# Kernel optimization log

Hardware: AMD Instinct MI355X
Metric: run time of the kernel (lower is better)

Reference implementation:

```python
import jax, jax.numpy as jnp
import numpy as np

N = 10000       # atoms
E = 160000      # edges
F = 128         # node_dim
NB = 20         # num radial basis
BLOCKS = 3      # action_blocks
CUTOFF = 5.0
ZMAX = 100
EPS = 1e-8


def _layernorm(x, g, b):
    mu = jnp.mean(x, axis=-1, keepdims=True)
    var = jnp.var(x, axis=-1, keepdims=True)
    return (x - mu) * jax.lax.rsqrt(var + 1e-5) * g + b


def setup_inputs() -> dict:
    key = jax.random.key(0)
    ks = jax.random.split(key, 16)
    W = 0.05  # weight init scale, keeps activations stable over 3 blocks
    inp = {
        "pos": jax.random.uniform(ks[0], (N, 3), dtype=jnp.float32),
        "z": jax.random.randint(ks[1], (N,), 0, ZMAX),
        "edge_index": jax.random.randint(ks[2], (2, E), 0, N),
        "z_embed": jax.random.normal(ks[3], (ZMAX, F), dtype=jnp.float32),
        "Wrbf": jax.random.normal(ks[4], (BLOCKS, NB, 3 * F), dtype=jnp.float32) * W,
        "brbf": jnp.zeros((BLOCKS, 3 * F), jnp.float32),
        "ln_g": jnp.ones((BLOCKS, F), jnp.float32),
        "ln_b": jnp.zeros((BLOCKS, F), jnp.float32),
        "Wm1": jax.random.normal(ks[5], (BLOCKS, F, F), dtype=jnp.float32) * W,
        "bm1": jnp.zeros((BLOCKS, F), jnp.float32),
        "Wm2": jax.random.normal(ks[6], (BLOCKS, F, 3 * F), dtype=jnp.float32) * W,
        "bm2": jnp.zeros((BLOCKS, 3 * F), jnp.float32),
        "Uw": jax.random.normal(ks[7], (BLOCKS, F, F), dtype=jnp.float32) * W,
        "Vw": jax.random.normal(ks[8], (BLOCKS, F, F), dtype=jnp.float32) * W,
        "ln2_g": jnp.ones((BLOCKS, F), jnp.float32),
        "ln2_b": jnp.zeros((BLOCKS, F), jnp.float32),
        "Wu1": jax.random.normal(ks[9], (BLOCKS, 2 * F, F), dtype=jnp.float32) * W,
        "bu1": jnp.zeros((BLOCKS, F), jnp.float32),
        "Wu2": jax.random.normal(ks[10], (BLOCKS, F, 3 * F), dtype=jnp.float32) * W,
        "bu2": jnp.zeros((BLOCKS, 3 * F), jnp.float32),
        "Wo1": jax.random.normal(ks[11], (F, F), dtype=jnp.float32) * W,
        "bo1": jnp.zeros((F,), jnp.float32),
        "Wo2": jax.random.normal(ks[12], (F, 1), dtype=jnp.float32) * W,
        "bo2": jnp.zeros((1,), jnp.float32),
    }
    return inp


def _forward(pos, z, edge_index, z_embed, Wrbf, brbf, ln_g, ln_b, Wm1, bm1,
             Wm2, bm2, Uw, Vw, ln2_g, ln2_b, Wu1, bu1, Wu2, bu2,
             Wo1, bo1, Wo2, bo2):
    src, dst = edge_index[0], edge_index[1]
    # ---- edge data: distances, bessel RBF, cosine cutoff ----
    rvec = pos[dst] - pos[src]                          # [E,3]
    d = jnp.sqrt(jnp.sum(rvec * rvec, axis=-1) + EPS)   # [E]
    rhat = rvec / d[:, None]                            # [E,3]
    n = jnp.arange(1, NB + 1, dtype=jnp.float32)
    rbf = jnp.sin(n[None, :] * jnp.pi * d[:, None] / CUTOFF) / d[:, None]  # [E,NB]
    fc = jnp.where(d < CUTOFF, 0.5 * (jnp.cos(jnp.pi * d / CUTOFF) + 1.0), 0.0)
    # ---- embedding ----
    x = z_embed[z]                                      # [N,F] scalar features
    v = jnp.zeros((x.shape[0], 3, F), x.dtype)          # [N,3,F] vector features
    nseg = x.shape[0]
    for b in range(BLOCKS):
        # ---- message block (PaiNN) ----
        xn = _layernorm(x, ln_g[b], ln_b[b])
        phi = jax.nn.silu(xn @ Wm1[b] + bm1[b]) @ Wm2[b] + bm2[b]          # [N,3F]
        Wf = (rbf @ Wrbf[b] + brbf[b]) * fc[:, None]                       # [E,3F]
        m = phi[src] * Wf                                                  # [E,3F]
        ms, mvv, mvs = m[:, :F], m[:, F:2 * F], m[:, 2 * F:]
        dx = jax.ops.segment_sum(ms, dst, num_segments=nseg)               # [N,F]
        ev = mvv[:, None, :] * v[src] + mvs[:, None, :] * rhat[:, :, None] # [E,3,F]
        dv = jax.ops.segment_sum(ev, dst, num_segments=nseg)               # [N,3,F]
        x = x + dx
        v = v + dv
        # ---- update block (PaiNN) ----
        Uv = jnp.einsum('ncf,fg->ncg', v, Uw[b])
        Vv = jnp.einsum('ncf,fg->ncg', v, Vw[b])
        vnorm = jnp.sqrt(jnp.sum(Vv * Vv, axis=1) + EPS)                   # [N,F]
        xn2 = _layernorm(x, ln2_g[b], ln2_b[b])
        a = jax.nn.silu(jnp.concatenate([xn2, vnorm], -1) @ Wu1[b] + bu1[b]) @ Wu2[b] + bu2[b]
        avv, asv, ass = a[:, :F], a[:, F:2 * F], a[:, 2 * F:]
        x = x + asv * jnp.sum(Uv * Vv, axis=1) + ass
        v = v + avv[:, None, :] * Uv
    # ---- energy output head ----
    e_atom = jax.nn.silu(x @ Wo1 + bo1) @ Wo2 + bo2                        # [N,1]
    return jnp.sum(e_atom)


def reference(pos, z, edge_index, z_embed, Wrbf, brbf, ln_g, ln_b, Wm1, bm1,
              Wm2, bm2, Uw, Vw, ln2_g, ln2_b, Wu1, bu1, Wu2, bu2,
              Wo1, bo1, Wo2, bo2):
    return _forward(pos, z, edge_index, z_embed, Wrbf, brbf, ln_g, ln_b,
                    Wm1, bm1, Wm2, bm2, Uw, Vw, ln2_g, ln2_b,
                    Wu1, bu1, Wu2, bu2, Wo1, bo1, Wo2, bo2)
```

## Files before the change

kernel.cpp:

```cpp
#include <hip/hip_runtime.h>
#include <math.h>

#define N_ATOM 10000
#define NEDGE  160000
#define F      128
#define F3     384
#define NB     20
#define NBLK   3
#define PI_F   3.14159265358979323846f

__device__ __forceinline__ float silu_f(float x){ return x / (1.0f + __expf(-x)); }

__global__ __launch_bounds__(256) void k_init(const float* __restrict__ z_embed,
                                              const int* __restrict__ z,
                                              float* __restrict__ x, float* __restrict__ v){
  int idx = blockIdx.x * 256 + threadIdx.x;
  if (idx < N_ATOM * F){
    int i = idx >> 7, f = idx & 127;
    x[idx] = z_embed[z[i] * F + f];
  }
  if (idx < N_ATOM * 3 * F) v[idx] = 0.0f;
}

__global__ __launch_bounds__(256) void k_hist(const int* __restrict__ ei, int* __restrict__ deg){
  int e = blockIdx.x * 256 + threadIdx.x;
  atomicAdd(&deg[ei[NEDGE + e]], 1);
}

__global__ __launch_bounds__(1024) void k_scan(const int* __restrict__ deg,
                                               int* __restrict__ rowptr, int* __restrict__ cursor){
  __shared__ int part[1024];
  int t = threadIdx.x;
  int base = t * 10;
  int loc[10];
  int s = 0;
  #pragma unroll
  for (int i = 0; i < 10; i++){
    int idx = base + i;
    int d = (idx < N_ATOM) ? deg[idx] : 0;
    loc[i] = s; s += d;
  }
  part[t] = s;
  __syncthreads();
  for (int off = 1; off < 1024; off <<= 1){
    int vp = 0;
    if (t >= off) vp = part[t - off];
    __syncthreads();
    part[t] += vp;
    __syncthreads();
  }
  int offset = (t == 0) ? 0 : part[t - 1];
  #pragma unroll
  for (int i = 0; i < 10; i++){
    int idx = base + i;
    if (idx < N_ATOM){ rowptr[idx] = offset + loc[i]; cursor[idx] = offset + loc[i]; }
  }
  if (t == 1023) rowptr[N_ATOM] = part[1023];
}

__global__ __launch_bounds__(256) void k_slot(const int* __restrict__ ei,
                                              int* __restrict__ cursor, int* __restrict__ slot){
  int e = blockIdx.x * 256 + threadIdx.x;
  int p = atomicAdd(&cursor[ei[NEDGE + e]], 1);
  slot[e] = p;
}

__global__ __launch_bounds__(256) void k_geo(const float* __restrict__ pos,
                                             const int* __restrict__ ei,
                                             const int* __restrict__ slot,
                                             int* __restrict__ srcs,
                                             float* __restrict__ rhs,
                                             float* __restrict__ rbfs,
                                             float* __restrict__ fcs){
  int e = blockIdx.x * 256 + threadIdx.x;
  int s = ei[e], d_ = ei[NEDGE + e];
  int p = slot[e];
  float rx = pos[d_*3+0] - pos[s*3+0];
  float ry = pos[d_*3+1] - pos[s*3+1];
  float rz = pos[d_*3+2] - pos[s*3+2];
  float d  = sqrtf(rx*rx + ry*ry + rz*rz + 1e-8f);
  float inv = 1.0f / d;
  srcs[p] = s;
  rhs[p*3+0] = rx*inv; rhs[p*3+1] = ry*inv; rhs[p*3+2] = rz*inv;
  float fcv = (d < 5.0f) ? 0.5f * (cosf(PI_F * d * 0.2f) + 1.0f) : 0.0f;
  fcs[p] = fcv;
  float base = PI_F * d * 0.2f;
  float sc = inv * fcv;
  #pragma unroll
  for (int k = 0; k < NB; k++){
    rbfs[(size_t)p*NB + k] = sinf(base * (float)(k+1)) * sc;
  }
}

__global__ __launch_bounds__(256) void k_node_phi(const float* __restrict__ x,
                                                  float* __restrict__ phi,
                                                  const float* __restrict__ ln_g, const float* __restrict__ ln_b,
                                                  const float* __restrict__ Wm1, const float* __restrict__ bm1,
                                                  const float* __restrict__ Wm2, const float* __restrict__ bm2){
  __shared__ float xn[16][F];
  __shared__ float h [16][F];
  __shared__ float mu_s[16], rs_s[16];
  int t = threadIdx.x;
  int row0 = blockIdx.x * 16;

  {
    int r = t >> 4, l = t & 15;
    const float* xr = x + (size_t)(row0 + r) * F;
    float s = 0.f, ss = 0.f;
    #pragma unroll
    for (int i = 0; i < 8; i++){ float vv = xr[l + 16*i]; s += vv; ss += vv*vv; }
    #pragma unroll
    for (int m = 8; m >= 1; m >>= 1){ s += __shfl_xor(s, m, 64); ss += __shfl_xor(ss, m, 64); }
    if (l == 0){
      float mu = s * (1.0f/F);
      float var = ss * (1.0f/F) - mu*mu;
      mu_s[r] = mu; rs_s[r] = rsqrtf(var + 1e-5f);
    }
  }
  __syncthreads();
  #pragma unroll
  for (int i = 0; i < 8; i++){
    int idx = t + 256*i; int r = idx >> 7, f = idx & 127;
    float vv = x[(size_t)(row0 + r)*F + f];
    xn[r][f] = (vv - mu_s[r]) * rs_s[r] * ln_g[f] + ln_b[f];
  }
  __syncthreads();
  {
    int c = t & 127, grp = t >> 7;
    float acc[8];
    #pragma unroll
    for (int i = 0; i < 8; i++) acc[i] = bm1[c];
    for (int k = 0; k < F; k++){
      float w = Wm1[k*F + c];
      #pragma unroll
      for (int i = 0; i < 8; i++) acc[i] += xn[grp*8 + i][k] * w;
    }
    #pragma unroll
    for (int i = 0; i < 8; i++) h[grp*8 + i][c] = silu_f(acc[i]);
  }
  __syncthreads();
  {
    int j = t & 127, grp = t >> 7;
    float a0[8], a1[8], a2[8];
    #pragma unroll
    for (int i = 0; i < 8; i++){ a0[i] = bm2[j]; a1[i] = bm2[128+j]; a2[i] = bm2[256+j]; }
    for (int k = 0; k < F; k++){
      float w0 = Wm2[k*F3 + j], w1 = Wm2[k*F3 + 128 + j], w2 = Wm2[k*F3 + 256 + j];
      #pragma unroll
      for (int i = 0; i < 8; i++){
        float hv = h[grp*8 + i][k];
        a0[i] += hv*w0; a1[i] += hv*w1; a2[i] += hv*w2;
      }
    }
    #pragma unroll
    for (int i = 0; i < 8; i++){
      size_t row = row0 + grp*8 + i;
      phi[row*F3 + j]       = a0[i];
      phi[row*F3 + 128 + j] = a1[i];
      phi[row*F3 + 256 + j] = a2[i];
    }
  }
}

__global__ __launch_bounds__(256) void k_edge_g(const int* __restrict__ rowptr,
                                                const int* __restrict__ srcs,
                                                const float* __restrict__ rbfs,
                                                const float* __restrict__ rhs,
                                                const float* __restrict__ fcs,
                                                const float* __restrict__ phi,
                                                const float* __restrict__ v,
                                                const float* __restrict__ Wrbf,
                                                const float* __restrict__ brbf,
                                                float* __restrict__ x,
                                                float* __restrict__ vnew){
  __shared__ float W[NB * F3];
  int t = threadIdx.x;
  #pragma unroll
  for (int i = 0; i < (NB*F3)/256; i++) W[t + 256*i] = Wrbf[t + 256*i];
  __syncthreads();

  int wid = t >> 6, lane = t & 63;
  int n = blockIdx.x * 4 + wid;
  int f0 = lane, f1 = lane + 64;
  int r0 = rowptr[n], r1 = rowptr[n+1];

  float bs0  = brbf[f0],       bs1  = brbf[f1];
  float bvv0 = brbf[F + f0],   bvv1 = brbf[F + f1];
  float bvs0 = brbf[2*F + f0], bvs1 = brbf[2*F + f1];

  float ax0=0.f, ax1=0.f;
  float av00=0.f, av01=0.f, av10=0.f, av11=0.f, av20=0.f, av21=0.f;

  for (int j = r0; j < r1; ++j){
    int s = srcs[j];
    float fcv = fcs[j];
    float rh0 = rhs[j*3+0], rh1 = rhs[j*3+1], rh2 = rhs[j*3+2];
    const float* rb = rbfs + (size_t)j * NB;
    float w_s0=0.f, w_s1=0.f, wvv0=0.f, wvv1=0.f, wvs0=0.f, wvs1=0.f;
    #pragma unroll
    for (int k = 0; k < NB; k++){
      float r = rb[k];
      w_s0 += r * W[k*F3 + f0];        w_s1 += r * W[k*F3 + f1];
      wvv0 += r * W[k*F3 + F + f0];    wvv1 += r * W[k*F3 + F + f1];
      wvs0 += r * W[k*F3 + 2*F + f0];  wvs1 += r * W[k*F3 + 2*F + f1];
    }
    const float* ps = phi + (size_t)s * F3;
    const float* vs = v   + (size_t)s * 3 * F;
    float ms0  = ps[f0]       * (w_s0 + bs0 *fcv);
    float ms1  = ps[f1]       * (w_s1 + bs1 *fcv);
    float mvv0 = ps[F + f0]   * (wvv0 + bvv0*fcv);
    float mvv1 = ps[F + f1]   * (wvv1 + bvv1*fcv);
    float mvs0 = ps[2*F + f0] * (wvs0 + bvs0*fcv);
    float mvs1 = ps[2*F + f1] * (wvs1 + bvs1*fcv);
    ax0 += ms0; ax1 += ms1;
    av00 += mvv0*vs[f0]       + mvs0*rh0;  av01 += mvv1*vs[f1]       + mvs1*rh0;
    av10 += mvv0*vs[F + f0]   + mvs0*rh1;  av11 += mvv1*vs[F + f1]   + mvs1*rh1;
    av20 += mvv0*vs[2*F + f0] + mvs0*rh2;  av21 += mvv1*vs[2*F + f1] + mvs1*rh2;
  }

  size_t xb = (size_t)n * F;
  x[xb + f0] += ax0;  x[xb + f1] += ax1;
  size_t vb = (size_t)n * 3 * F;
  vnew[vb + f0]       = v[vb + f0]       + av00;  vnew[vb + f1]       = v[vb + f1]       + av01;
  vnew[vb + F + f0]   = v[vb + F + f0]   + av10;  vnew[vb + F + f1]   = v[vb + F + f1]   + av11;
  vnew[vb + 2*F + f0] = v[vb + 2*F + f0] + av20;  vnew[vb + 2*F + f1] = v[vb + 2*F + f1] + av21;
}

__global__ __launch_bounds__(256) void k_node_upd(float* __restrict__ x, float* __restrict__ v,
                                                  const float* __restrict__ vnew,
                                                  const float* __restrict__ Uw, const float* __restrict__ Vw,
                                                  const float* __restrict__ ln2_g, const float* __restrict__ ln2_b,
                                                  const float* __restrict__ Wu1, const float* __restrict__ bu1,
                                                  const float* __restrict__ Wu2, const float* __restrict__ bu2){
  __shared__ float vn [8][3][F];
  __shared__ float Uvs[8][3][F];
  __shared__ float xl [8][F];
  __shared__ float xn2[8][F];
  __shared__ float vno[8][F];
  __shared__ float duv[8][F];
  __shared__ float hl [8][F];
  __shared__ float mu_s[8], rs_s[8];
  int t = threadIdx.x;
  int n0 = blockIdx.x * 8;

  #pragma unroll
  for (int i = 0; i < 12; i++){
    int idx = t + 256*i;
    ((float*)vn)[idx] = vnew[(size_t)n0*3*F + idx];
  }
  #pragma unroll
  for (int i = 0; i < 4; i++){
    int idx = t + 256*i;
    ((float*)xl)[idx] = x[(size_t)n0*F + idx];
  }
  __syncthreads();

  {
    int r = t >> 5, l = t & 31;
    float s = 0.f, ss = 0.f;
    #pragma unroll
    for (int i = 0; i < 4; i++){ float vv = xl[r][l + 32*i]; s += vv; ss += vv*vv; }
    #pragma unroll
    for (int m = 16; m >= 1; m >>= 1){ s += __shfl_xor(s, m, 64); ss += __shfl_xor(ss, m, 64); }
    if (l == 0){ float mu = s*(1.0f/F); mu_s[r] = mu; rs_s[r] = rsqrtf(ss*(1.0f/F) - mu*mu + 1e-5f); }
  }
  __syncthreads();
  #pragma unroll
  for (int i = 0; i < 4; i++){
    int idx = t + 256*i; int r = idx >> 7, f = idx & 127;
    xn2[r][f] = (xl[r][f] - mu_s[r]) * rs_s[r] * ln2_g[f] + ln2_b[f];
  }

  {
    int g = t & 127, grp = t >> 7;
    float au[12], av[12];
    #pragma unroll
    for (int p = 0; p < 12; p++){ au[p]=0.f; av[p]=0.f; }
    for (int k = 0; k < F; k++){
      float uw = Uw[k*F + g], vw = Vw[k*F + g];
      #pragma unroll
      for (int n = 0; n < 4; n++){
        #pragma unroll
        for (int c = 0; c < 3; c++){
          float vv = vn[grp*4 + n][c][k];
          au[n*3+c] += vv*uw; av[n*3+c] += vv*vw;
        }
      }
    }
    #pragma unroll
    for (int n = 0; n < 4; n++){
      float v0 = av[n*3+0], v1 = av[n*3+1], v2 = av[n*3+2];
      float u0 = au[n*3+0], u1 = au[n*3+1], u2 = au[n*3+2];
      vno[grp*4+n][g] = sqrtf(v0*v0 + v1*v1 + v2*v2 + 1e-8f);
      duv[grp*4+n][g] = u0*v0 + u1*v1 + u2*v2;
      Uvs[grp*4+n][0][g] = u0; Uvs[grp*4+n][1][g] = u1; Uvs[grp*4+n][2][g] = u2;
    }
  }
  __syncthreads();

  {
    int g = t & 127, grp = t >> 7;
    float acc[4];
    #pragma unroll
    for (int n = 0; n < 4; n++) acc[n] = bu1[g];
    for (int k = 0; k < F; k++){
      float w = Wu1[k*F + g];
      #pragma unroll
      for (int n = 0; n < 4; n++) acc[n] += xn2[grp*4+n][k] * w;
    }
    for (int k = 0; k < F; k++){
      float w = Wu1[(F + k)*F + g];
      #pragma unroll
      for (int n = 0; n < 4; n++) acc[n] += vno[grp*4+n][k] * w;
    }
    #pragma unroll
    for (int n = 0; n < 4; n++) hl[grp*4+n][g] = silu_f(acc[n]);
  }
  __syncthreads();

  {
    int f = t & 127, grp = t >> 7;
    float a0[4], a1[4], a2[4];
    #pragma unroll
    for (int n = 0; n < 4; n++){ a0[n] = bu2[f]; a1[n] = bu2[128+f]; a2[n] = bu2[256+f]; }
    for (int k = 0; k < F; k++){
      float w0 = Wu2[k*F3 + f], w1 = Wu2[k*F3 + 128 + f], w2 = Wu2[k*F3 + 256 + f];
      #pragma unroll
      for (int n = 0; n < 4; n++){
        float hv = hl[grp*4+n][k];
        a0[n] += hv*w0; a1[n] += hv*w1; a2[n] += hv*w2;
      }
    }
    #pragma unroll
    for (int n = 0; n < 4; n++){
      int nl = grp*4 + n;
      size_t row = n0 + nl;
      x[row*F + f] = xl[nl][f] + a1[n]*duv[nl][f] + a2[n];
      #pragma unroll
      for (int c = 0; c < 3; c++)
        v[(row*3 + c)*F + f] = vn[nl][c][f] + a0[n]*Uvs[nl][c][f];
    }
  }
}

__global__ __launch_bounds__(256) void k_out(const float* __restrict__ x,
                                             const float* __restrict__ Wo1, const float* __restrict__ bo1,
                                             const float* __restrict__ Wo2, const float* __restrict__ bo2,
                                             float* __restrict__ out){
  __shared__ float xl[8][F];
  __shared__ float hl[8][F];
  __shared__ float er[8];
  int t = threadIdx.x; int n0 = blockIdx.x * 8;
  #pragma unroll
  for (int i = 0; i < 4; i++){ int idx = t + 256*i; ((float*)xl)[idx] = x[(size_t)n0*F + idx]; }
  __syncthreads();
  { int g = t & 127, grp = t >> 7;
    float acc[4];
    #pragma unroll
    for (int n = 0; n < 4; n++) acc[n] = bo1[g];
    for (int k = 0; k < F; k++){
      float w = Wo1[k*F + g];
      #pragma unroll
      for (int n = 0; n < 4; n++) acc[n] += xl[grp*4+n][k] * w;
    }
    #pragma unroll
    for (int n = 0; n < 4; n++) hl[grp*4+n][g] = silu_f(acc[n]);
  }
  __syncthreads();
  { int r = t >> 5, l = t & 31;
    float s = 0.f;
    #pragma unroll
    for (int i = 0; i < 4; i++) s += hl[r][l + 32*i] * Wo2[l + 32*i];
    #pragma unroll
    for (int m = 16; m >= 1; m >>= 1) s += __shfl_xor(s, m, 64);
    if (l == 0) er[r] = s + bo2[0];
  }
  __syncthreads();
  if (t == 0){
    float s = 0.f;
    #pragma unroll
    for (int r = 0; r < 8; r++) s += er[r];
    unsafeAtomicAdd(out, s);
  }
}

extern "C" void kernel_launch(void* const* d_in, const int* in_sizes, int n_in,
                              void* d_out, int out_size, void* d_ws, size_t ws_size,
                              hipStream_t stream){
  const float* pos     = (const float*)d_in[0];
  const int*   z       = (const int*)  d_in[1];
  const int*   ei      = (const int*)  d_in[2];
  const float* z_embed = (const float*)d_in[3];
  const float* Wrbf    = (const float*)d_in[4];
  const float* brbf    = (const float*)d_in[5];
  const float* ln_g    = (const float*)d_in[6];
  const float* ln_b    = (const float*)d_in[7];
  const float* Wm1     = (const float*)d_in[8];
  const float* bm1     = (const float*)d_in[9];
  const float* Wm2     = (const float*)d_in[10];
  const float* bm2     = (const float*)d_in[11];
  const float* Uw      = (const float*)d_in[12];
  const float* Vw      = (const float*)d_in[13];
  const float* ln2_g   = (const float*)d_in[14];
  const float* ln2_b   = (const float*)d_in[15];
  const float* Wu1     = (const float*)d_in[16];
  const float* bu1     = (const float*)d_in[17];
  const float* Wu2     = (const float*)d_in[18];
  const float* bu2     = (const float*)d_in[19];
  const float* Wo1     = (const float*)d_in[20];
  const float* bo1     = (const float*)d_in[21];
  const float* Wo2     = (const float*)d_in[22];
  const float* bo2     = (const float*)d_in[23];

  float* ws = (float*)d_ws;
  size_t o = 0;
  float* x     = ws + o; o += (size_t)N_ATOM * F;
  float* v     = ws + o; o += (size_t)N_ATOM * 3 * F;
  float* phi   = ws + o; o += (size_t)N_ATOM * 3 * F;
  float* vnew  = ws + o; o += (size_t)N_ATOM * 3 * F;
  float* rhs   = ws + o; o += (size_t)NEDGE * 3;
  float* rbfs  = ws + o; o += (size_t)NEDGE * NB;
  float* fcs   = ws + o; o += (size_t)NEDGE;
  int*   rowptr= (int*)(ws + o); o += N_ATOM + 16;
  int*   srcs  = (int*)(ws + o); o += NEDGE;
  int* deg    = (int*)vnew;
  int* cursor = deg + 10240;
  int* slot   = cursor + 10240;

  hipMemsetAsync(d_out, 0, sizeof(float), stream);
  hipMemsetAsync(deg, 0, N_ATOM * sizeof(int), stream);
  k_hist<<<NEDGE/256, 256, 0, stream>>>(ei, deg);
  k_scan<<<1, 1024, 0, stream>>>(deg, rowptr, cursor);
  k_slot<<<NEDGE/256, 256, 0, stream>>>(ei, cursor, slot);
  k_geo <<<NEDGE/256, 256, 0, stream>>>(pos, ei, slot, srcs, rhs, rbfs, fcs);
  k_init<<<(N_ATOM*3*F + 255)/256, 256, 0, stream>>>(z_embed, z, x, v);

  for (int b = 0; b < NBLK; b++){
    k_node_phi<<<N_ATOM/16, 256, 0, stream>>>(x, phi,
        ln_g + b*F, ln_b + b*F, Wm1 + (size_t)b*F*F, bm1 + b*F,
        Wm2 + (size_t)b*F*F3, bm2 + b*F3);
    k_edge_g<<<N_ATOM/4, 256, 0, stream>>>(rowptr, srcs, rbfs, rhs, fcs,
        phi, v, Wrbf + (size_t)b*NB*F3, brbf + b*F3, x, vnew);
    k_node_upd<<<N_ATOM/8, 256, 0, stream>>>(x, v, vnew,
        Uw + (size_t)b*F*F, Vw + (size_t)b*F*F,
        ln2_g + b*F, ln2_b + b*F,
        Wu1 + (size_t)b*2*F*F, bu1 + b*F,
        Wu2 + (size_t)b*F*F3, bu2 + b*F3);
  }
  k_out<<<N_ATOM/8, 256, 0, stream>>>(x, Wo1, bo1, Wo2, bo2, (float*)d_out);
}
```

Baseline: 785.4 us.

## Use bf16 MFMA for node MLPs with pre-transposed bf16 weights

Rewrites k_node_phi and k_node_upd so their dense matmuls run on 16x16x32 bf16 MFMA instructions instead of scalar FP32 FMA loops. A new prep kernel converts and transposes the weights to bf16 once per call. Tiles grow to 64 rows for phi and 16 nodes for update, with shared-memory layouts padded to 136 and 264. Activations such as Uv, Vv and duv are kept in bf16 in shared memory, which lowers precision relative to the FP32 reference.

```diff
diff --git a/kernel.cpp b/kernel.cpp
--- a/kernel.cpp
+++ b/kernel.cpp
@@ -9,7 +9,56 @@
 #define NBLK   3
 #define PI_F   3.14159265358979323846f
 
+typedef __attribute__((ext_vector_type(8))) short bf16x8;
+typedef __attribute__((ext_vector_type(4))) float f32x4;
+#define MFMA16(a,b,c) __builtin_amdgcn_mfma_f32_16x16x32_bf16(a,b,c,0,0,0)
+
 __device__ __forceinline__ float silu_f(float x){ return x / (1.0f + __expf(-x)); }
+__device__ __forceinline__ short f2b(float f){
+  unsigned u = __float_as_uint(f);
+  u += 0x7fff + ((u >> 16) & 1);
+  return (short)(u >> 16);
+}
+__device__ __forceinline__ float b2f(short s){
+  return __uint_as_float(((unsigned)(unsigned short)s) << 16);
+}
+
+__global__ __launch_bounds__(256) void k_prep(const float* __restrict__ Wm1, const float* __restrict__ Wm2,
+                                              const float* __restrict__ Uw,  const float* __restrict__ Vw,
+                                              const float* __restrict__ Wu1, const float* __restrict__ Wu2,
+                                              short* __restrict__ wt){
+  int idx = blockIdx.x * 256 + threadIdx.x;
+  short* wm1t = wt;
+  short* wm2t = wt + 49152;
+  short* uwt  = wt + 196608;
+  short* vwt  = wt + 245760;
+  short* wu1t = wt + 294912;
+  short* wu2t = wt + 393216;
+  if (idx < 49152){
+    int b = idx >> 14, r = idx & 16383, n = r >> 7, k = r & 127;
+    wm1t[idx] = f2b(Wm1[b*16384 + k*128 + n]);
+  } else if (idx < 196608){
+    int j = idx - 49152;
+    int b = j / 49152, r = j % 49152, n = r >> 7, k = r & 127;
+    wm2t[j] = f2b(Wm2[b*49152 + k*384 + n]);
+  } else if (idx < 245760){
+    int j = idx - 196608;
+    int b = j >> 14, r = j & 16383, n = r >> 7, k = r & 127;
+    uwt[j] = f2b(Uw[b*16384 + k*128 + n]);
+  } else if (idx < 294912){
+    int j = idx - 245760;
+    int b = j >> 14, r = j & 16383, n = r >> 7, k = r & 127;
+    vwt[j] = f2b(Vw[b*16384 + k*128 + n]);
+  } else if (idx < 393216){
+    int j = idx - 294912;
+    int b = j >> 15, r = j & 32767, n = r >> 8, k = r & 255;
+    wu1t[j] = f2b(Wu1[b*32768 + k*128 + n]);
+  } else if (idx < 540672){
+    int j = idx - 393216;
+    int b = j / 49152, r = j % 49152, n = r >> 7, k = r & 127;
+    wu2t[j] = f2b(Wu2[b*49152 + k*384 + n]);
+  }
+}
 
 __global__ __launch_bounds__(256) void k_init(const float* __restrict__ z_embed,
                                               const int* __restrict__ z,
@@ -95,69 +144,77 @@
 __global__ __launch_bounds__(256) void k_node_phi(const float* __restrict__ x,
                                                   float* __restrict__ phi,
                                                   const float* __restrict__ ln_g, const float* __restrict__ ln_b,
-                                                  const float* __restrict__ Wm1, const float* __restrict__ bm1,
-                                                  const float* __restrict__ Wm2, const float* __restrict__ bm2){
-  __shared__ float xn[16][F];
-  __shared__ float h [16][F];
-  __shared__ float mu_s[16], rs_s[16];
+                                                  const short* __restrict__ Wm1t, const float* __restrict__ bm1,
+                                                  const short* __restrict__ Wm2t, const float* __restrict__ bm2){
+  __shared__ short xn_s[64*136];
+  __shared__ short h_s [64*136];
+  __shared__ float mu_s[64], rs_s[64];
   int t = threadIdx.x;
-  int row0 = blockIdx.x * 16;
-
-  {
-    int r = t >> 4, l = t & 15;
+  int row0 = blockIdx.x * 64; if (row0 > N_ATOM - 64) row0 = N_ATOM - 64;
+
+  {
+    int r = t >> 2, q = t & 3;
     const float* xr = x + (size_t)(row0 + r) * F;
     float s = 0.f, ss = 0.f;
     #pragma unroll
-    for (int i = 0; i < 8; i++){ float vv = xr[l + 16*i]; s += vv; ss += vv*vv; }
-    #pragma unroll
-    for (int m = 8; m >= 1; m >>= 1){ s += __shfl_xor(s, m, 64); ss += __shfl_xor(ss, m, 64); }
-    if (l == 0){
+    for (int i = 0; i < 32; i++){ float vv = xr[q + 4*i]; s += vv; ss += vv*vv; }
+    s += __shfl_xor(s, 1, 64); ss += __shfl_xor(ss, 1, 64);
+    s += __shfl_xor(s, 2, 64); ss += __shfl_xor(ss, 2, 64);
+    if (q == 0){
       float mu = s * (1.0f/F);
-      float var = ss * (1.0f/F) - mu*mu;
-      mu_s[r] = mu; rs_s[r] = rsqrtf(var + 1e-5f);
-    }
-  }
-  __syncthreads();
-  #pragma unroll
-  for (int i = 0; i < 8; i++){
+      mu_s[r] = mu; rs_s[r] = rsqrtf(ss * (1.0f/F) - mu*mu + 1e-5f);
+    }
+  }
+  __syncthreads();
+  #pragma unroll
+  for (int i = 0; i < 32; i++){
     int idx = t + 256*i; int r = idx >> 7, f = idx & 127;
     float vv = x[(size_t)(row0 + r)*F + f];
-    xn[r][f] = (vv - mu_s[r]) * rs_s[r] * ln_g[f] + ln_b[f];
-  }
-  __syncthreads();
-  {
-    int c = t & 127, grp = t >> 7;
-    float acc[8];
-    #pragma unroll
-    for (int i = 0; i < 8; i++) acc[i] = bm1[c];
-    for (int k = 0; k < F; k++){
-      float w = Wm1[k*F + c];
-      #pragma unroll
-      for (int i = 0; i < 8; i++) acc[i] += xn[grp*8 + i][k] * w;
-    }
-    #pragma unroll
-    for (int i = 0; i < 8; i++) h[grp*8 + i][c] = silu_f(acc[i]);
-  }
-  __syncthreads();
-  {
-    int j = t & 127, grp = t >> 7;
-    float a0[8], a1[8], a2[8];
-    #pragma unroll
-    for (int i = 0; i < 8; i++){ a0[i] = bm2[j]; a1[i] = bm2[128+j]; a2[i] = bm2[256+j]; }
-    for (int k = 0; k < F; k++){
-      float w0 = Wm2[k*F3 + j], w1 = Wm2[k*F3 + 128 + j], w2 = Wm2[k*F3 + 256 + j];
-      #pragma unroll
-      for (int i = 0; i < 8; i++){
-        float hv = h[grp*8 + i][k];
-        a0[i] += hv*w0; a1[i] += hv*w1; a2[i] += hv*w2;
+    xn_s[r*136 + f] = f2b((vv - mu_s[r]) * rs_s[r] * ln_g[f] + ln_b[f]);
+  }
+  __syncthreads();
+
+  int l = t & 63, w = t >> 6;
+  int wr0  = w * 16;
+  int arow = wr0 + (l & 15);
+  int kof  = (l >> 4) * 8;
+  int drow = wr0 + (l >> 4) * 4;
+
+  {
+    bf16x8 af[4];
+    #pragma unroll
+    for (int ks = 0; ks < 4; ks++) af[ks] = *(const bf16x8*)&xn_s[arow*136 + ks*32 + kof];
+    #pragma unroll
+    for (int ct = 0; ct < 8; ct++){
+      int col = ct*16 + (l & 15);
+      float bb = bm1[col];
+      f32x4 acc = {bb, bb, bb, bb};
+      #pragma unroll
+      for (int ks = 0; ks < 4; ks++){
+        bf16x8 bf = *(const bf16x8*)&Wm1t[col*F + ks*32 + kof];
+        acc = MFMA16(af[ks], bf, acc);
       }
-    }
-    #pragma unroll
-    for (int i = 0; i < 8; i++){
-      size_t row = row0 + grp*8 + i;
-      phi[row*F3 + j]       = a0[i];
-      phi[row*F3 + 128 + j] = a1[i];
-      phi[row*F3 + 256 + j] = a2[i];
+      #pragma unroll
+      for (int i = 0; i < 4; i++) h_s[(drow + i)*136 + col] = f2b(silu_f(acc[i]));
+    }
+  }
+  __syncthreads();
+  {
+    bf16x8 af[4];
+    #pragma unroll
+    for (int ks = 0; ks < 4; ks++) af[ks] = *(const bf16x8*)&h_s[arow*136 + ks*32 + kof];
+    #pragma unroll
+    for (int ct = 0; ct < 24; ct++){
+      int col = ct*16 + (l & 15);
+      float bb = bm2[col];
+      f32x4 acc = {bb, bb, bb, bb};
+      #pragma unroll
+      for (int ks = 0; ks < 4; ks++){
+        bf16x8 bf = *(const bf16x8*)&Wm2t[col*F + ks*32 + kof];
+        acc = MFMA16(af[ks], bf, acc);
+      }
+      #pragma unroll
+      for (int i = 0; i < 4; i++) phi[(size_t)(row0 + drow + i)*F3 + col] = acc[i];
     }
   }
 }
@@ -228,117 +285,137 @@
 
 __global__ __launch_bounds__(256) void k_node_upd(float* __restrict__ x, float* __restrict__ v,
                                                   const float* __restrict__ vnew,
-                                                  const float* __restrict__ Uw, const float* __restrict__ Vw,
+                                                  const short* __restrict__ Uwt, const short* __restrict__ Vwt,
                                                   const float* __restrict__ ln2_g, const float* __restrict__ ln2_b,
-                                                  const float* __restrict__ Wu1, const float* __restrict__ bu1,
-                                                  const float* __restrict__ Wu2, const float* __restrict__ bu2){
-  __shared__ float vn [8][3][F];
-  __shared__ float Uvs[8][3][F];
-  __shared__ float xl [8][F];
-  __shared__ float xn2[8][F];
-  __shared__ float vno[8][F];
-  __shared__ float duv[8][F];
-  __shared__ float hl [8][F];
-  __shared__ float mu_s[8], rs_s[8];
+                                                  const short* __restrict__ Wu1t, const float* __restrict__ bu1,
+                                                  const short* __restrict__ Wu2t, const float* __restrict__ bu2){
+  __shared__ __align__(16) char smem[59776];
+  short* vt   = (short*)smem;
+  short* Uv_s = (short*)(smem + 13056);
+  char*  R    = smem + 26112;
+  short* Vv_s = (short*)R;
+  short* ab   = (short*)(R + 13056);
+  float* a_s  = (float*)R;
+  short* h2   = (short*)(smem + 50688);
+  short* duv  = (short*)(smem + 55040);
+  float* mu_s = (float*)(smem + 59392);
+  float* rs_s = mu_s + 16;
+
   int t = threadIdx.x;
-  int n0 = blockIdx.x * 8;
-
-  #pragma unroll
-  for (int i = 0; i < 12; i++){
-    int idx = t + 256*i;
-    ((float*)vn)[idx] = vnew[(size_t)n0*3*F + idx];
-  }
-  #pragma unroll
-  for (int i = 0; i < 4; i++){
-    int idx = t + 256*i;
-    ((float*)xl)[idx] = x[(size_t)n0*F + idx];
-  }
-  __syncthreads();
-
-  {
-    int r = t >> 5, l = t & 31;
+  int n0 = blockIdx.x * 16;
+
+  {
+    int r = t >> 4, q = t & 15;
+    const float* xr = x + (size_t)(n0 + r) * F;
     float s = 0.f, ss = 0.f;
     #pragma unroll
-    for (int i = 0; i < 4; i++){ float vv = xl[r][l + 32*i]; s += vv; ss += vv*vv; }
-    #pragma unroll
-    for (int m = 16; m >= 1; m >>= 1){ s += __shfl_xor(s, m, 64); ss += __shfl_xor(ss, m, 64); }
-    if (l == 0){ float mu = s*(1.0f/F); mu_s[r] = mu; rs_s[r] = rsqrtf(ss*(1.0f/F) - mu*mu + 1e-5f); }
-  }
-  __syncthreads();
-  #pragma unroll
-  for (int i = 0; i < 4; i++){
-    int idx = t + 256*i; int r = idx >> 7, f = idx & 127;
-    xn2[r][f] = (xl[r][f] - mu_s[r]) * rs_s[r] * ln2_g[f] + ln2_b[f];
-  }
-
-  {
-    int g = t & 127, grp = t >> 7;
-    float au[12], av[12];
-    #pragma unroll
-    for (int p = 0; p < 12; p++){ au[p]=0.f; av[p]=0.f; }
-    for (int k = 0; k < F; k++){
-      float uw = Uw[k*F + g], vw = Vw[k*F + g];
-      #pragma unroll
-      for (int n = 0; n < 4; n++){
+    for (int i = 0; i < 8; i++){ float vv = xr[q + 16*i]; s += vv; ss += vv*vv; }
+    #pragma unroll
+    for (int m = 8; m >= 1; m >>= 1){ s += __shfl_xor(s, m, 64); ss += __shfl_xor(ss, m, 64); }
+    if (q == 0){ float mu = s*(1.0f/F); mu_s[r] = mu; rs_s[r] = rsqrtf(ss*(1.0f/F) - mu*mu + 1e-5f); }
+  }
+  #pragma unroll
+  for (int i = 0; i < 24; i++){
+    int idx = t + 256*i; int row = idx >> 7, f = idx & 127;
+    vt[row*136 + f] = f2b(vnew[(size_t)(n0*3 + row)*F + f]);
+  }
+  __syncthreads();
+
+  int l = t & 63, w = t >> 6;
+  int kof = (l >> 4) * 8;
+
+  {
+    #pragma unroll
+    for (int jj = 0; jj < 3; jj++){
+      int job = w*3 + jj;
+      int rt = job >> 2, rem = job & 3, mat = rem >> 1, ch = rem & 1;
+      const short* Bt = mat ? Vwt : Uwt;
+      short* Out = mat ? Vv_s : Uv_s;
+      bf16x8 af[4];
+      #pragma unroll
+      for (int ks = 0; ks < 4; ks++) af[ks] = *(const bf16x8*)&vt[(rt*16 + (l&15))*136 + ks*32 + kof];
+      #pragma unroll
+      for (int ct = 0; ct < 4; ct++){
+        int col = ch*64 + ct*16 + (l & 15);
+        f32x4 acc = {0.f, 0.f, 0.f, 0.f};
         #pragma unroll
-        for (int c = 0; c < 3; c++){
-          float vv = vn[grp*4 + n][c][k];
-          au[n*3+c] += vv*uw; av[n*3+c] += vv*vw;
+        for (int ks = 0; ks < 4; ks++){
+          bf16x8 bf = *(const bf16x8*)&Bt[col*F + ks*32 + kof];
+          acc = MFMA16(af[ks], bf, acc);
         }
+        #pragma unroll
+        for (int i = 0; i < 4; i++) Out[(rt*16 + (l>>4)*4 + i)*136 + col] = f2b(acc[i]);
       }
     }
-    #pragma unroll
-    for (int n = 0; n < 4; n++){
-      float v0 = av[n*3+0], v1 = av[n*3+1], v2 = av[n*3+2];
-      float u0 = au[n*3+0], u1 = au[n*3+1], u2 = au[n*3+2];
-      vno[grp*4+n][g] = sqrtf(v0*v0 + v1*v1 + v2*v2 + 1e-8f);
-      duv[grp*4+n][g] = u0*v0 + u1*v1 + u2*v2;
-      Uvs[grp*4+n][0][g] = u0; Uvs[grp*4+n][1][g] = u1; Uvs[grp*4+n][2][g] = u2;
-    }
-  }
-  __syncthreads();
-
-  {
-    int g = t & 127, grp = t >> 7;
-    float acc[4];
-    #pragma unroll
-    for (int n = 0; n < 4; n++) acc[n] = bu1[g];
-    for (int k = 0; k < F; k++){
-      float w = Wu1[k*F + g];
-      #pragma unroll
-      for (int n = 0; n < 4; n++) acc[n] += xn2[grp*4+n][k] * w;
-    }
-    for (int k = 0; k < F; k++){
-      float w = Wu1[(F + k)*F + g];
-      #pragma unroll
-      for (int n = 0; n < 4; n++) acc[n] += vno[grp*4+n][k] * w;
-    }
-    #pragma unroll
-    for (int n = 0; n < 4; n++) hl[grp*4+n][g] = silu_f(acc[n]);
-  }
-  __syncthreads();
-
-  {
-    int f = t & 127, grp = t >> 7;
-    float a0[4], a1[4], a2[4];
-    #pragma unroll
-    for (int n = 0; n < 4; n++){ a0[n] = bu2[f]; a1[n] = bu2[128+f]; a2[n] = bu2[256+f]; }
-    for (int k = 0; k < F; k++){
-      float w0 = Wu2[k*F3 + f], w1 = Wu2[k*F3 + 128 + f], w2 = Wu2[k*F3 + 256 + f];
-      #pragma unroll
-      for (int n = 0; n < 4; n++){
-        float hv = hl[grp*4+n][k];
-        a0[n] += hv*w0; a1[n] += hv*w1; a2[n] += hv*w2;
+  }
+  __syncthreads();
+
+  {
+    #pragma unroll
+    for (int i = 0; i < 8; i++){
+      int idx = t + 256*i; int n = idx >> 7, f = idx & 127;
+      float xv = x[(size_t)(n0 + n)*F + f];
+      ab[n*264 + f] = f2b((xv - mu_s[n]) * rs_s[n] * ln2_g[f] + ln2_b[f]);
+      float v0 = b2f(Vv_s[(3*n+0)*136 + f]), v1 = b2f(Vv_s[(3*n+1)*136 + f]), v2 = b2f(Vv_s[(3*n+2)*136 + f]);
+      float u0 = b2f(Uv_s[(3*n+0)*136 + f]), u1 = b2f(Uv_s[(3*n+1)*136 + f]), u2 = b2f(Uv_s[(3*n+2)*136 + f]);
+      ab[n*264 + 128 + f] = f2b(sqrtf(v0*v0 + v1*v1 + v2*v2 + 1e-8f));
+      duv[n*136 + f] = f2b(u0*v0 + u1*v1 + u2*v2);
+    }
+  }
+  __syncthreads();
+
+  {
+    bf16x8 af[8];
+    #pragma unroll
+    for (int ks = 0; ks < 8; ks++) af[ks] = *(const bf16x8*)&ab[(l&15)*264 + ks*32 + kof];
+    #pragma unroll
+    for (int cc = 0; cc < 2; cc++){
+      int col = (w*2 + cc)*16 + (l & 15);
+      float bb = bu1[col];
+      f32x4 acc = {bb, bb, bb, bb};
+      #pragma unroll
+      for (int ks = 0; ks < 8; ks++){
+        bf16x8 bf = *(const bf16x8*)&Wu1t[col*256 + ks*32 + kof];
+        acc = MFMA16(af[ks], bf, acc);
       }
-    }
-    #pragma unroll
-    for (int n = 0; n < 4; n++){
-      int nl = grp*4 + n;
-      size_t row = n0 + nl;
-      x[row*F + f] = xl[nl][f] + a1[n]*duv[nl][f] + a2[n];
-      #pragma unroll
-      for (int c = 0; c < 3; c++)
-        v[(row*3 + c)*F + f] = vn[nl][c][f] + a0[n]*Uvs[nl][c][f];
+      #pragma unroll
+      for (int i = 0; i < 4; i++) h2[((l>>4)*4 + i)*136 + col] = f2b(silu_f(acc[i]));
+    }
+  }
+  __syncthreads();
+
+  {
+    bf16x8 af[4];
+    #pragma unroll
+    for (int ks = 0; ks < 4; ks++) af[ks] = *(const bf16x8*)&h2[(l&15)*136 + ks*32 + kof];
+    #pragma unroll
+    for (int cc = 0; cc < 6; cc++){
+      int col = (w*6 + cc)*16 + (l & 15);
+      float bb = bu2[col];
+      f32x4 acc = {bb, bb, bb, bb};
+      #pragma unroll
+      for (int ks = 0; ks < 4; ks++){
+        bf16x8 bf = *(const bf16x8*)&Wu2t[col*F + ks*32 + kof];
+        acc = MFMA16(af[ks], bf, acc);
+      }
+      #pragma unroll
+      for (int i = 0; i < 4; i++) a_s[((l>>4)*4 + i)*384 + col] = acc[i];
+    }
+  }
+  __syncthreads();
+
+  {
+    #pragma unroll
+    for (int i = 0; i < 8; i++){
+      int idx = t + 256*i; int n = idx >> 7, f = idx & 127;
+      float avv = a_s[n*384 + f], asv = a_s[n*384 + 128 + f], ass = a_s[n*384 + 256 + f];
+      size_t xr_ = (size_t)(n0 + n)*F + f;
+      x[xr_] = x[xr_] + asv * b2f(duv[n*136 + f]) + ass;
+      #pragma unroll
+      for (int c = 0; c < 3; c++){
+        size_t vr = (size_t)((n0 + n)*3 + c)*F + f;
+        v[vr] = vnew[vr] + avv * b2f(Uv_s[(3*n + c)*136 + f]);
+      }
     }
   }
 }
@@ -367,13 +444,13 @@
     for (int n = 0; n < 4; n++) hl[grp*4+n][g] = silu_f(acc[n]);
   }
   __syncthreads();
-  { int r = t >> 5, l = t & 31;
+  { int r = t >> 5, lq = t & 31;
     float s = 0.f;
     #pragma unroll
-    for (int i = 0; i < 4; i++) s += hl[r][l + 32*i] * Wo2[l + 32*i];
+    for (int i = 0; i < 4; i++) s += hl[r][lq + 32*i] * Wo2[lq + 32*i];
     #pragma unroll
     for (int m = 16; m >= 1; m >>= 1) s += __shfl_xor(s, m, 64);
-    if (l == 0) er[r] = s + bo2[0];
+    if (lq == 0) er[r] = s + bo2[0];
   }
   __syncthreads();
   if (t == 0){
@@ -423,12 +500,21 @@
   float* fcs   = ws + o; o += (size_t)NEDGE;
   int*   rowptr= (int*)(ws + o); o += N_ATOM + 16;
   int*   srcs  = (int*)(ws + o); o += NEDGE;
+  short* wt    = (short*)(ws + o); o += 270336 + 8;
   int* deg    = (int*)vnew;
   int* cursor = deg + 10240;
   int* slot   = cursor + 10240;
 
+  short* wm1t = wt;
+  short* wm2t = wt + 49152;
+  short* uwt  = wt + 196608;
+  short* vwt  = wt + 245760;
+  short* wu1t = wt + 294912;
+  short* wu2t = wt + 393216;
+
   hipMemsetAsync(d_out, 0, sizeof(float), stream);
   hipMemsetAsync(deg, 0, N_ATOM * sizeof(int), stream);
+  k_prep<<<2112, 256, 0, stream>>>(Wm1, Wm2, Uw, Vw, Wu1, Wu2, wt);
   k_hist<<<NEDGE/256, 256, 0, stream>>>(ei, deg);
   k_scan<<<1, 1024, 0, stream>>>(deg, rowptr, cursor);
   k_slot<<<NEDGE/256, 256, 0, stream>>>(ei, cursor, slot);
@@ -436,16 +522,16 @@
   k_init<<<(N_ATOM*3*F + 255)/256, 256, 0, stream>>>(z_embed, z, x, v);
 
   for (int b = 0; b < NBLK; b++){
-    k_node_phi<<<N_ATOM/16, 256, 0, stream>>>(x, phi,
-        ln_g + b*F, ln_b + b*F, Wm1 + (size_t)b*F*F, bm1 + b*F,
-        Wm2 + (size_t)b*F*F3, bm2 + b*F3);
+    k_node_phi<<<157, 256, 0, stream>>>(x, phi,
+        ln_g + b*F, ln_b + b*F, wm1t + b*16384, bm1 + b*F,
+        wm2t + b*49152, bm2 + b*F3);
     k_edge_g<<<N_ATOM/4, 256, 0, stream>>>(rowptr, srcs, rbfs, rhs, fcs,
         phi, v, Wrbf + (size_t)b*NB*F3, brbf + b*F3, x, vnew);
-    k_node_upd<<<N_ATOM/8, 256, 0, stream>>>(x, v, vnew,
-        Uw + (size_t)b*F*F, Vw + (size_t)b*F*F,
+    k_node_upd<<<N_ATOM/16, 256, 0, stream>>>(x, v, vnew,
+        uwt + b*16384, vwt + b*16384,
         ln2_g + b*F, ln2_b + b*F,
-        Wu1 + (size_t)b*2*F*F, bu1 + b*F,
-        Wu2 + (size_t)b*F*F3, bu2 + b*F3);
+        wu1t + b*32768, bu1 + b*F,
+        wu2t + b*49152, bu2 + b*F3);
   }
   k_out<<<N_ATOM/8, 256, 0, stream>>>(x, Wo1, bo1, Wo2, bo2, (float*)d_out);
 }
```

Measured after the change: 689.8 us. 12.2% less time.
